# Optimization experiments

Hardware: AMD Instinct MI355X
Metric: run time of the kernel (lower is better)

The kernel has to match this reference:

```python
import jax, jax.numpy as jnp
import numpy as np
import math

B, T, C = 4, 2048, 1024
D_ATTN, N_HEAD = 1024, 16
HEAD = D_ATTN // N_HEAD


def setup_inputs() -> dict:
    key = jax.random.key(0)
    k1, k2, k3 = jax.random.split(key, 3)
    x = jax.random.normal(k1, (B, T, C), dtype=jnp.float32)
    mask = jnp.tril(jnp.ones((T, T), dtype=jnp.int32))  # causal mask, 0 = blocked
    W_qkv = jax.random.normal(k2, (C, 3 * D_ATTN), dtype=jnp.float32) * (1.0 / math.sqrt(C))
    b_qkv = jnp.zeros((3 * D_ATTN,), dtype=jnp.float32)
    W_out = jax.random.normal(k3, (D_ATTN, C), dtype=jnp.float32) * (1.0 / math.sqrt(D_ATTN))
    b_out = jnp.zeros((C,), dtype=jnp.float32)
    return {"x": x, "mask": mask, "W_qkv": W_qkv, "b_qkv": b_qkv, "W_out": W_out, "b_out": b_out}


def reference(x, mask, W_qkv, b_qkv, W_out, b_out):
    Bx, Tx, Cx = x.shape
    qkv = x @ W_qkv + b_qkv                      # [B, T, 3*d_attn]
    q, k, v = jnp.split(qkv, 3, axis=-1)
    # [B, T, d_attn] -> [B, H, T, head]
    q = q.reshape(Bx, Tx, N_HEAD, HEAD).transpose(0, 2, 1, 3)
    k = k.reshape(Bx, Tx, N_HEAD, HEAD).transpose(0, 2, 1, 3)
    v = v.reshape(Bx, Tx, N_HEAD, HEAD).transpose(0, 2, 1, 3)
    scale = 1.0 / math.sqrt(HEAD)
    scores = jnp.einsum('bhqd,bhkd->bhqk', q, k) * scale  # [B, H, T, T]
    scores = jnp.where(mask == 0, -jnp.inf, scores)
    att = jax.nn.softmax(scores, axis=-1)
    out = jnp.einsum('bhqk,bhkd->bhqd', att, v)           # [B, H, T, head]
    out = out.transpose(0, 2, 1, 3).reshape(Bx, Tx, D_ATTN)
    return out @ W_out + b_out
```

## Files before the change

kernel.cpp:

```cpp
#include <hip/hip_runtime.h>

#define B_    4
#define T_    2048
#define C_    1024
#define DATTN 1024
#define NHEAD 16
#define M_    (B_*T_)
#define NQKV  (3*DATTN)

typedef __bf16 bf16;
typedef bf16  bf16x8 __attribute__((ext_vector_type(8)));
typedef float f32x4  __attribute__((ext_vector_type(4)));
typedef unsigned short u16x8 __attribute__((ext_vector_type(8)));

#define NEGBIG (-1e30f)

typedef const __attribute__((address_space(1))) unsigned int* gas_u32;
typedef __attribute__((address_space(3))) unsigned int* las_u32;

__global__ void detect_dtype(const unsigned short* __restrict__ x, int* flag) {
    __shared__ int cnt;
    if (threadIdx.x == 0) cnt = 0;
    __syncthreads();
    int local = 0;
    for (int j = 0; j < 8; ++j) {
        u16x8 v = *(const u16x8*)&x[(j * 256 + threadIdx.x) * 8];
        for (int k = 0; k < 8; ++k)
            if ((v[k] & 0x7F80) == 0x7F80) ++local;
    }
    atomicAdd(&cnt, local);
    __syncthreads();
    if (threadIdx.x == 0) *flag = (cnt > 0) ? 1 : 0;
}

__global__ void convert_x_any(const void* __restrict__ src, bf16* __restrict__ dst,
                              int n, const int* __restrict__ flag) {
    int i = (blockIdx.x * 256 + threadIdx.x) * 8;
    if (i >= n) return;
    if (*flag == 0) {
        *(bf16x8*)&dst[i] = *(const bf16x8*)((const bf16*)src + i);
    } else {
        const float* s = (const float*)src + i;
        f32x4 a = *(const f32x4*)s, b2 = *(const f32x4*)(s + 4);
        bf16x8 r;
        r[0] = (bf16)a[0]; r[1] = (bf16)a[1]; r[2] = (bf16)a[2]; r[3] = (bf16)a[3];
        r[4] = (bf16)b2[0]; r[5] = (bf16)b2[1]; r[6] = (bf16)b2[2]; r[7] = (bf16)b2[3];
        *(bf16x8*)&dst[i] = r;
    }
}

__global__ void prep_bias(const void* __restrict__ bq, const void* __restrict__ bo,
                          bf16* __restrict__ dq, bf16* __restrict__ do_,
                          const int* __restrict__ flag) {
    const int f = *flag;
    int i = blockIdx.x * 256 + threadIdx.x;
    if (i < NQKV)
        dq[i] = f ? (bf16)((const float*)bq)[i] : ((const bf16*)bq)[i];
    else if (i - NQKV < C_)
        do_[i - NQKV] = f ? (bf16)((const float*)bo)[i - NQKV] : ((const bf16*)bo)[i - NQKV];
}

__global__ void transpose_w_any(const void* __restrict__ src, bf16* __restrict__ dst,
                                int R, int C, const int* __restrict__ flag) {
    __shared__ bf16 tile[32][33];
    const int f = *flag;
    const int c0 = blockIdx.x * 32, r0 = blockIdx.y * 32;
    const int tx = threadIdx.x & 31, ty = threadIdx.x >> 5;
    for (int p = 0; p < 4; ++p) {
        int row = p * 8 + ty;
        size_t idx = (size_t)(r0 + row) * C + c0 + tx;
        float v = f ? ((const float*)src)[idx] : (float)((const bf16*)src)[idx];
        tile[row][tx] = (bf16)v;
    }
    __syncthreads();
    for (int p = 0; p < 4; ++p) {
        int row = p * 8 + ty;
        dst[(size_t)(c0 + row) * R + r0 + tx] = tile[tx][row];
    }
}

__global__ void transpose_v(const bf16* __restrict__ qkv, bf16* __restrict__ vt) {
    __shared__ bf16 tile[32][33];
    const int t0 = blockIdx.x * 32, d0 = blockIdx.y * 32, bh = blockIdx.z;
    const int b = bh >> 4, h = bh & 15;
    const int tx = threadIdx.x & 31, ty = threadIdx.x >> 5;
    for (int p = 0; p < 4; ++p) {
        int tt = p * 8 + ty;
        tile[tt][tx] = qkv[((size_t)b * T_ + t0 + tt) * NQKV + 2 * DATTN + h * 64 + d0 + tx];
    }
    __syncthreads();
    for (int p = 0; p < 4; ++p) {
        int dd = p * 8 + ty;
        vt[((size_t)bh * 64 + d0 + dd) * T_ + t0 + tx] = tile[tx][dd];
    }
}

template<typename TC>
__global__ __launch_bounds__(256) void gemm_bt(const bf16* __restrict__ A,
                                               const bf16* __restrict__ Bt,
                                               const bf16* __restrict__ bias,
                                               TC* __restrict__ Cc,
                                               int M, int N, int K,
                                               const int* __restrict__ flag, int want) {
    if (flag && *flag != want) return;
    __shared__ __align__(16) bf16 As[128 * 64];
    __shared__ __align__(16) bf16 Bs[128 * 64];
    const int tid  = threadIdx.x;
    const int lane = tid & 63, wave = tid >> 6;
    const int quad = lane >> 4, l15 = lane & 15;
    const int wr = wave >> 1, wc = wave & 1;
    const int m0 = blockIdx.y * 128, n0 = blockIdx.x * 128;
    const int srow = lane >> 3;
    const int scol = ((lane & 7) ^ srow) * 8;
    const int l7x8 = (l15 & 7);

    f32x4 acc[4][4];
    for (int i = 0; i < 4; ++i)
        for (int j = 0; j < 4; ++j)
            acc[i][j] = f32x4{0.f, 0.f, 0.f, 0.f};

    for (int k0 = 0; k0 < K; k0 += 64) {
        for (int c = 0; c < 4; ++c) {
            int chunk = wave * 4 + c;
            int row = chunk * 8 + srow;
            __builtin_amdgcn_global_load_lds(
                (gas_u32)&A[(size_t)(m0 + row) * K + k0 + scol],
                (las_u32)&As[chunk * 512], 16, 0, 0);
            __builtin_amdgcn_global_load_lds(
                (gas_u32)&Bt[(size_t)(n0 + row) * K + k0 + scol],
                (las_u32)&Bs[chunk * 512], 16, 0, 0);
        }
        __syncthreads();
        for (int ks = 0; ks < 2; ++ks) {
            bf16x8 af[4], bfr[4];
            for (int i = 0; i < 4; ++i)
                af[i] = *(const bf16x8*)&As[(wr * 64 + i * 16 + l15) * 64 +
                                            (((ks * 4 + quad) ^ l7x8) * 8)];
            for (int j = 0; j < 4; ++j)
                bfr[j] = *(const bf16x8*)&Bs[(wc * 64 + j * 16 + l15) * 64 +
                                             (((ks * 4 + quad) ^ l7x8) * 8)];
            for (int i = 0; i < 4; ++i)
                for (int j = 0; j < 4; ++j)
                    acc[i][j] = __builtin_amdgcn_mfma_f32_16x16x32_bf16(af[i], bfr[j], acc[i][j], 0, 0, 0);
        }
        __syncthreads();
    }

    for (int i = 0; i < 4; ++i) {
        int row = m0 + wr * 64 + i * 16 + quad * 4;
        for (int j = 0; j < 4; ++j) {
            int col = n0 + wc * 64 + j * 16 + l15;
            float bv = (float)bias[col];
            for (int r = 0; r < 4; ++r) {
                float v = acc[i][j][r] + bv;
                if constexpr (__is_same(TC, float)) Cc[(size_t)(row + r) * N + col] = v;
                else                                Cc[(size_t)(row + r) * N + col] = (bf16)v;
            }
        }
    }
}

__global__ __launch_bounds__(256) void attn_fused6(const bf16* __restrict__ qkv,
                                                   const bf16* __restrict__ vt,
                                                   bf16* __restrict__ out) {
    __shared__ __align__(16) bf16 Ks[2][64 * 64];
    __shared__ __align__(16) bf16 Vs[2][64 * 64];
    __shared__ __align__(16) bf16 Ps[2 * 4 * 16 * 72];
    const int tid  = threadIdx.x;
    const int lane = tid & 63, wave = tid >> 6;
    const int quad = lane >> 4, l15 = lane & 15;
    const int srow = lane >> 3;
    const int scol = ((lane & 7) ^ srow) * 8;
    const int l7x8 = (l15 & 7);
    const int bh = blockIdx.x & 63;
    const int i  = blockIdx.x >> 6;
    const int b  = bh >> 4, h = bh & 15;
    const int lo = i, hi = 31 - i;
    const size_t rowbase = (size_t)b * T_;
    const float SC = 0.125f * 1.44269504088896f;

    auto stage = [&](int kt, int buf) {
        const int k0 = kt * 64;
        for (int p = 0; p < 2; ++p) {
            int chunk = wave * 2 + p;
            int row = chunk * 8 + srow;
            __builtin_amdgcn_global_load_lds(
                (gas_u32)&qkv[(rowbase + k0 + row) * NQKV + DATTN + h * 64 + scol],
                (las_u32)&Ks[buf][chunk * 512], 16, 0, 0);
            __builtin_amdgcn_global_load_lds(
                (gas_u32)&vt[((size_t)bh * 64 + row) * T_ + k0 + scol],
                (las_u32)&Vs[buf][chunk * 512], 16, 0, 0);
        }
    };

    bf16x8 qf[2][2];
#pragma unroll
    for (int t = 0; t < 2; ++t) {
        int q0 = (t ? hi : lo) * 64;
        size_t r = rowbase + q0 + wave * 16 + l15;
        const bf16* p = &qkv[r * NQKV + h * 64];
        qf[t][0] = *(const bf16x8*)&p[quad * 8];
        qf[t][1] = *(const bf16x8*)&p[32 + quad * 8];
    }

    f32x4 oa[2][4];
    float lacc[2][4];
#pragma unroll
    for (int t = 0; t < 2; ++t)
        for (int c = 0; c < 4; ++c) {
            oa[t][c] = f32x4{0.f, 0.f, 0.f, 0.f};
            lacc[t][c] = 0.f;
        }

    bf16* Pw0 = &Ps[(0 * 4 + wave) * 16 * 72];
    bf16* Pw1 = &Ps[(1 * 4 + wave) * 16 * 72];

    stage(0, 0);

    for (int kt = 0; kt <= hi; ++kt) {
        const int k0 = kt * 64;
        const bool act0 = (kt <= lo);
        const int buf = kt & 1;
        __syncthreads();
        if (kt < hi) stage(kt + 1, buf ^ 1);

        const bf16* Kb = Ks[buf];
        const bf16* Vb = Vs[buf];

        f32x4 s0[4], s1[4];
        for (int c = 0; c < 4; ++c) {
            s0[c] = f32x4{0.f, 0.f, 0.f, 0.f};
            s1[c] = f32x4{0.f, 0.f, 0.f, 0.f};
        }
        for (int ks = 0; ks < 2; ++ks)
            for (int c = 0; c < 4; ++c) {
                bf16x8 kf = *(const bf16x8*)&Kb[(c * 16 + l15) * 64 +
                                                (((ks * 4 + quad) ^ l7x8) * 8)];
                if (act0) s0[c] = __builtin_amdgcn_mfma_f32_16x16x32_bf16(qf[0][ks], kf, s0[c], 0, 0, 0);
                s1[c] = __builtin_amdgcn_mfma_f32_16x16x32_bf16(qf[1][ks], kf, s1[c], 0, 0, 0);
            }

#pragma unroll
        for (int t = 0; t < 2; ++t) {
            if (t == 0 && !act0) continue;
            const int q0 = (t ? hi : lo) * 64;
            const bool diag = (kt == (t ? hi : lo));
            bf16* Pw = t ? Pw1 : Pw0;
            for (int c = 0; c < 4; ++c) {
                int key = k0 + c * 16 + l15;
                for (int r = 0; r < 4; ++r) {
                    float v = (t ? s1[c][r] : s0[c][r]) * SC;
                    if (diag && key > q0 + wave * 16 + quad * 4 + r) v = NEGBIG;
                    float p = __builtin_amdgcn_exp2f(v);
                    lacc[t][r] += p;
                    Pw[(quad * 4 + r) * 72 + c * 16 + l15] = (bf16)p;
                }
            }
        }

        for (int ks2 = 0; ks2 < 2; ++ks2) {
            bf16x8 pf0{}, pf1;
            if (act0) pf0 = *(const bf16x8*)&Pw0[l15 * 72 + ks2 * 32 + quad * 8];
            pf1 = *(const bf16x8*)&Pw1[l15 * 72 + ks2 * 32 + quad * 8];
            for (int c2 = 0; c2 < 4; ++c2) {
                bf16x8 vf = *(const bf16x8*)&Vb[(c2 * 16 + l15) * 64 +
                                                (((ks2 * 4 + quad) ^ l7x8) * 8)];
                if (act0) oa[0][c2] = __builtin_amdgcn_mfma_f32_16x16x32_bf16(pf0, vf, oa[0][c2], 0, 0, 0);
                oa[1][c2] = __builtin_amdgcn_mfma_f32_16x16x32_bf16(pf1, vf, oa[1][c2], 0, 0, 0);
            }
        }
    }

#pragma unroll
    for (int t = 0; t < 2; ++t) {
        int q0 = (t ? hi : lo) * 64;
        float inv[4];
        for (int r = 0; r < 4; ++r) {
            float v = lacc[t][r];
            for (int off = 1; off < 16; off <<= 1) v += __shfl_xor(v, off);
            inv[r] = 1.f / v;
        }
        size_t r0 = rowbase + q0 + wave * 16 + quad * 4;
        for (int c2 = 0; c2 < 4; ++c2) {
            int col = h * 64 + c2 * 16 + l15;
            for (int r = 0; r < 4; ++r)
                out[(r0 + r) * (size_t)DATTN + col] = (bf16)(oa[t][c2][r] * inv[r]);
        }
    }
}

extern "C" void kernel_launch(void* const* d_in, const int* in_sizes, int n_in,
                              void* d_out, int out_size, void* d_ws, size_t ws_size,
                              hipStream_t stream) {
    const void* x     = d_in[0];
    const void* W_qkv = d_in[2];
    const void* b_qkv = d_in[3];
    const void* W_out = d_in[4];
    const void* b_out = d_in[5];

    char* ws = (char*)d_ws;
    int*  flag    = (int*)ws;
    bf16* qkv_buf = (bf16*)(ws + 256);
    bf16* Wqkv_t  = (bf16*)(ws + 256 + 50331648);
    bf16* Wout_t  = (bf16*)(ws + 256 + 56623104);
    bf16* att_buf = (bf16*)(ws + 256 + 58720256);
    bf16* vt_buf  = (bf16*)(ws + 256 + 75497472);
    bf16* x_bf    = (bf16*)(ws + 256 + 92274688);
    bf16* bq_bf   = (bf16*)(ws + 256 + 109051904);
    bf16* bo_bf   = (bf16*)(ws + 256 + 109058048);

    detect_dtype<<<1, 256, 0, stream>>>((const unsigned short*)x, flag);

    convert_x_any<<<M_ * C_ / (256 * 8), 256, 0, stream>>>(x, x_bf, M_ * C_, flag);
    prep_bias<<<(NQKV + C_) / 256, 256, 0, stream>>>(b_qkv, b_out, bq_bf, bo_bf, flag);
    transpose_w_any<<<dim3(NQKV / 32, C_ / 32), 256, 0, stream>>>(W_qkv, Wqkv_t, C_, NQKV, flag);
    transpose_w_any<<<dim3(C_ / 32, DATTN / 32), 256, 0, stream>>>(W_out, Wout_t, DATTN, C_, flag);

    gemm_bt<bf16><<<dim3(NQKV / 128, M_ / 128), 256, 0, stream>>>(
        x_bf, Wqkv_t, bq_bf, qkv_buf, M_, NQKV, C_, nullptr, 0);

    transpose_v<<<dim3(T_ / 32, 2, B_ * NHEAD), 256, 0, stream>>>(qkv_buf, vt_buf);

    attn_fused6<<<dim3(B_ * NHEAD * 16), 256, 0, stream>>>(qkv_buf, vt_buf, att_buf);

    gemm_bt<bf16 ><<<dim3(C_ / 128, M_ / 128), 256, 0, stream>>>(
        att_buf, Wout_t, bo_bf, (bf16*)d_out, M_, C_, DATTN, flag, 0);
    gemm_bt<float><<<dim3(C_ / 128, M_ / 128), 256, 0, stream>>>(
        att_buf, Wout_t, bo_bf, (float*)d_out, M_, C_, DATTN, flag, 1);
}
```

Before: 317.4 us.

## Keep attention probabilities in registers by computing transposed scores

The QK^T MFMA now takes its operands in swapped order, so the score accumulator comes out transposed. Each lane can then pack its exp2 probabilities straight into bf16x4 A-operands for a 16x16x16 MFMA on the PV product, with no round trip through LDS. This removes the P shared-memory buffer, its stores and reloads, and shrinks the row-sum reduction to two shuffles. In exchange it uses the smaller-K MFMA with 4-element V loads, adds inline asm for the bf16 pack, and sets launch_bounds to 4 blocks per CU, which adds register pressure.

Result: faster. 280.0 us (-11.8%).

```diff
diff --git a/kernel.cpp b/kernel.cpp
--- a/kernel.cpp
+++ b/kernel.cpp
@@ -10,6 +10,8 @@
 
 typedef __bf16 bf16;
 typedef bf16  bf16x8 __attribute__((ext_vector_type(8)));
+typedef bf16  bf16x4 __attribute__((ext_vector_type(4)));
+typedef short s16x4  __attribute__((ext_vector_type(4)));
 typedef float f32x4  __attribute__((ext_vector_type(4)));
 typedef unsigned short u16x8 __attribute__((ext_vector_type(8)));
 
@@ -17,6 +19,23 @@
 
 typedef const __attribute__((address_space(1))) unsigned int* gas_u32;
 typedef __attribute__((address_space(3))) unsigned int* las_u32;
+
+static __device__ __forceinline__ f32x4 mfma16(bf16x4 a, bf16x4 b, f32x4 c) {
+#if __has_builtin(__builtin_amdgcn_mfma_f32_16x16x16bf16_1k)
+    return __builtin_amdgcn_mfma_f32_16x16x16bf16_1k(
+        __builtin_bit_cast(s16x4, a), __builtin_bit_cast(s16x4, b), c, 0, 0, 0);
+#else
+    asm("v_mfma_f32_16x16x16_bf16 %0, %1, %2, %0" : "+v"(c) : "v"(a), "v"(b));
+    return c;
+#endif
+}
+
+static __device__ __forceinline__ bf16x4 pk4(float a, float b, float c, float d) {
+    union { unsigned int u[2]; bf16x4 v; } r;
+    asm("v_cvt_pk_bf16_f32 %0, %1, %2" : "=v"(r.u[0]) : "v"(a), "v"(b));
+    asm("v_cvt_pk_bf16_f32 %0, %1, %2" : "=v"(r.u[1]) : "v"(c), "v"(d));
+    return r.v;
+}
 
 __global__ void detect_dtype(const unsigned short* __restrict__ x, int* flag) {
     __shared__ int cnt;
@@ -160,18 +179,18 @@
     }
 }
 
-__global__ __launch_bounds__(256) void attn_fused6(const bf16* __restrict__ qkv,
-                                                   const bf16* __restrict__ vt,
-                                                   bf16* __restrict__ out) {
+__global__ __launch_bounds__(256, 4) void attn_fused7(const bf16* __restrict__ qkv,
+                                                      const bf16* __restrict__ vt,
+                                                      bf16* __restrict__ out) {
     __shared__ __align__(16) bf16 Ks[2][64 * 64];
     __shared__ __align__(16) bf16 Vs[2][64 * 64];
-    __shared__ __align__(16) bf16 Ps[2 * 4 * 16 * 72];
     const int tid  = threadIdx.x;
     const int lane = tid & 63, wave = tid >> 6;
     const int quad = lane >> 4, l15 = lane & 15;
     const int srow = lane >> 3;
     const int scol = ((lane & 7) ^ srow) * 8;
-    const int l7x8 = (l15 & 7);
+    const int l7   = l15 & 7;
+    const int g0   = quad >> 1, h4 = (quad & 1) * 4;
     const int bh = blockIdx.x & 63;
     const int i  = blockIdx.x >> 6;
     const int b  = bh >> 4, h = bh & 15;
@@ -204,16 +223,11 @@
     }
 
     f32x4 oa[2][4];
-    float lacc[2][4];
+    float lacc[2] = {0.f, 0.f};
 #pragma unroll
     for (int t = 0; t < 2; ++t)
-        for (int c = 0; c < 4; ++c) {
+        for (int c = 0; c < 4; ++c)
             oa[t][c] = f32x4{0.f, 0.f, 0.f, 0.f};
-            lacc[t][c] = 0.f;
-        }
-
-    bf16* Pw0 = &Ps[(0 * 4 + wave) * 16 * 72];
-    bf16* Pw1 = &Ps[(1 * 4 + wave) * 16 * 72];
 
     stage(0, 0);
 
@@ -228,61 +242,71 @@
         const bf16* Vb = Vs[buf];
 
         f32x4 s0[4], s1[4];
+#pragma unroll
         for (int c = 0; c < 4; ++c) {
             s0[c] = f32x4{0.f, 0.f, 0.f, 0.f};
             s1[c] = f32x4{0.f, 0.f, 0.f, 0.f};
         }
+#pragma unroll
         for (int ks = 0; ks < 2; ++ks)
+#pragma unroll
             for (int c = 0; c < 4; ++c) {
                 bf16x8 kf = *(const bf16x8*)&Kb[(c * 16 + l15) * 64 +
-                                                (((ks * 4 + quad) ^ l7x8) * 8)];
-                if (act0) s0[c] = __builtin_amdgcn_mfma_f32_16x16x32_bf16(qf[0][ks], kf, s0[c], 0, 0, 0);
-                s1[c] = __builtin_amdgcn_mfma_f32_16x16x32_bf16(qf[1][ks], kf, s1[c], 0, 0, 0);
+                                                (((ks * 4 + quad) ^ l7) * 8)];
+                if (act0) s0[c] = __builtin_amdgcn_mfma_f32_16x16x32_bf16(kf, qf[0][ks], s0[c], 0, 0, 0);
+                s1[c] = __builtin_amdgcn_mfma_f32_16x16x32_bf16(kf, qf[1][ks], s1[c], 0, 0, 0);
             }
 
+        bf16x4 paf[2][4];
 #pragma unroll
         for (int t = 0; t < 2; ++t) {
             if (t == 0 && !act0) continue;
             const int q0 = (t ? hi : lo) * 64;
             const bool diag = (kt == (t ? hi : lo));
-            bf16* Pw = t ? Pw1 : Pw0;
+            const int qa = q0 + wave * 16 + l15;
+            float lsum = 0.f;
+#pragma unroll
             for (int c = 0; c < 4; ++c) {
-                int key = k0 + c * 16 + l15;
+                const int keyb = k0 + c * 16 + quad * 4;
+                float pr[4];
+#pragma unroll
                 for (int r = 0; r < 4; ++r) {
                     float v = (t ? s1[c][r] : s0[c][r]) * SC;
-                    if (diag && key > q0 + wave * 16 + quad * 4 + r) v = NEGBIG;
+                    if (diag && keyb + r > qa) v = NEGBIG;
                     float p = __builtin_amdgcn_exp2f(v);
-                    lacc[t][r] += p;
-                    Pw[(quad * 4 + r) * 72 + c * 16 + l15] = (bf16)p;
+                    lsum += p;
+                    pr[r] = p;
                 }
+                paf[t][c] = pk4(pr[0], pr[1], pr[2], pr[3]);
             }
-        }
-
-        for (int ks2 = 0; ks2 < 2; ++ks2) {
-            bf16x8 pf0{}, pf1;
-            if (act0) pf0 = *(const bf16x8*)&Pw0[l15 * 72 + ks2 * 32 + quad * 8];
-            pf1 = *(const bf16x8*)&Pw1[l15 * 72 + ks2 * 32 + quad * 8];
+            lacc[t] += lsum;
+        }
+
+#pragma unroll
+        for (int c = 0; c < 4; ++c)
+#pragma unroll
             for (int c2 = 0; c2 < 4; ++c2) {
-                bf16x8 vf = *(const bf16x8*)&Vb[(c2 * 16 + l15) * 64 +
-                                                (((ks2 * 4 + quad) ^ l7x8) * 8)];
-                if (act0) oa[0][c2] = __builtin_amdgcn_mfma_f32_16x16x32_bf16(pf0, vf, oa[0][c2], 0, 0, 0);
-                oa[1][c2] = __builtin_amdgcn_mfma_f32_16x16x32_bf16(pf1, vf, oa[1][c2], 0, 0, 0);
+                bf16x4 vf = *(const bf16x4*)&Vb[(c2 * 16 + l15) * 64 +
+                                                (((2 * c + g0) ^ l7) * 8) + h4];
+                if (act0) oa[0][c2] = mfma16(paf[0][c], vf, oa[0][c2]);
+                oa[1][c2] = mfma16(paf[1][c], vf, oa[1][c2]);
             }
-        }
     }
 
 #pragma unroll
     for (int t = 0; t < 2; ++t) {
         int q0 = (t ? hi : lo) * 64;
+        float tot = lacc[t];
+        tot += __shfl_xor(tot, 16);
+        tot += __shfl_xor(tot, 32);
         float inv[4];
-        for (int r = 0; r < 4; ++r) {
-            float v = lacc[t][r];
-            for (int off = 1; off < 16; off <<= 1) v += __shfl_xor(v, off);
-            inv[r] = 1.f / v;
-        }
+#pragma unroll
+        for (int r = 0; r < 4; ++r) inv[r] = 1.f / __shfl(tot, quad * 4 + r);
         size_t r0 = rowbase + q0 + wave * 16 + quad * 4;
+#pragma unroll
         for (int c2 = 0; c2 < 4; ++c2) {
             int col = h * 64 + c2 * 16 + l15;
+#pragma unroll
             for (int r = 0; r < 4; ++r)
                 out[(r0 + r) * (size_t)DATTN + col] = (bf16)(oa[t][c2][r] * inv[r]);
         }
@@ -321,7 +345,7 @@
 
     transpose_v<<<dim3(T_ / 32, 2, B_ * NHEAD), 256, 0, stream>>>(qkv_buf, vt_buf);
 
-    attn_fused6<<<dim3(B_ * NHEAD * 16), 256, 0, stream>>>(qkv_buf, vt_buf, att_buf);
+    attn_fused7<<<dim3(B_ * NHEAD * 16), 256, 0, stream>>>(qkv_buf, vt_buf, att_buf);
 
     gemm_bt<bf16 ><<<dim3(C_ / 128, M_ / 128), 256, 0, stream>>>(
         att_buf, Wout_t, bo_bf, (bf16*)d_out, M_, C_, DATTN, flag, 0);
```
